# Optimization experiments

Measured on AMD Instinct MI355X. Metric: run time of the kernel, lower is better.

The kernel has to match this reference:

```python
import jax, jax.numpy as jnp
import numpy as np

S, I, H, FC, O = 16384, 64, 1024, 128, 1


def setup_inputs() -> dict:
    key = jax.random.key(0)
    ks = jax.random.split(key, 9)
    s_lstm = 1.0 / np.sqrt(H)
    return {
        "input_seq": jax.random.normal(ks[0], (S, I), jnp.float32),
        "W_ih": jax.random.uniform(ks[1], (4 * H, I), jnp.float32, -s_lstm, s_lstm),
        "W_hh": jax.random.uniform(ks[2], (4 * H, H), jnp.float32, -s_lstm, s_lstm),
        "b_ih": jax.random.uniform(ks[3], (4 * H,), jnp.float32, -s_lstm, s_lstm),
        "b_hh": jax.random.uniform(ks[4], (4 * H,), jnp.float32, -s_lstm, s_lstm),
        "fc1_w": jax.random.uniform(ks[5], (FC, H), jnp.float32, -s_lstm, s_lstm),
        "fc1_b": jax.random.uniform(ks[6], (FC,), jnp.float32, -s_lstm, s_lstm),
        "fc2_w": jax.random.uniform(ks[7], (O, FC), jnp.float32, -1.0 / np.sqrt(FC), 1.0 / np.sqrt(FC)),
        "fc2_b": jax.random.uniform(ks[8], (O,), jnp.float32, -1.0 / np.sqrt(FC), 1.0 / np.sqrt(FC)),
    }


def _lstm_scan(x, W_ih, W_hh, b_ih, b_hh):
    # PyTorch gate order: i, f, g, o. batch=1 collapsed; x: [S, I]
    xg = x @ W_ih.T + (b_ih + b_hh)  # precompute input-side gates: [S, 4H]

    def step(carry, xg_t):
        h, c = carry
        gates = xg_t + h @ W_hh.T
        i, f, g, o = jnp.split(gates, 4)
        i = jax.nn.sigmoid(i)
        f = jax.nn.sigmoid(f)
        g = jnp.tanh(g)
        o = jax.nn.sigmoid(o)
        c = f * c + i * g
        h = o * jnp.tanh(c)
        return (h, c), h

    h0 = jnp.zeros((H,), x.dtype)
    c0 = jnp.zeros((H,), x.dtype)
    _, hs = jax.lax.scan(step, (h0, c0), xg)
    return hs  # [S, H]


def reference(input_seq, W_ih, W_hh, b_ih, b_hh, fc1_w, fc1_b, fc2_w, fc2_b):
    hs = _lstm_scan(input_seq, W_ih, W_hh, b_ih, b_hh)       # [S, H]
    x = jax.nn.relu(hs)                                       # relu on LSTM outputs
    x = jax.nn.relu(x @ fc1_w.T + fc1_b)                      # [S, 128]
    x = x @ fc2_w.T + fc2_b                                   # [S, 1]
    return x[-1]                                              # [1]
```

## Files before the change

### kernel.cpp

```cpp
#include <hip/hip_runtime.h>
#include <hip/hip_fp16.h>


#define S_LEN 16384
#define I_DIM 64
#define H_DIM 1024
#define NBLK  64
#define NTHR  512

__device__ __forceinline__ float sigmoidf_(float x) { return 1.0f / (1.0f + __expf(-x)); }
__device__ __forceinline__ float tanh_fast(float x) { return 1.0f - 2.0f / (__expf(2.0f * x) + 1.0f); }
__device__ __forceinline__ float unpack_val(unsigned pk) {
    return __half2float(__ushort_as_half((unsigned short)(pk & 0xFFFFu)));
}

__global__ __launch_bounds__(NTHR, 2) void lstm_persistent(
    const float* __restrict__ xseq,
    const float* __restrict__ W_ih,
    const float* __restrict__ W_hh,
    const float* __restrict__ b_ih,
    const float* __restrict__ b_hh,
    unsigned* __restrict__ pairs)
{
    const int b    = blockIdx.x;
    const int tid  = threadIdx.x;
    const int w    = tid >> 6;
    const int c    = tid & 63;
    const int colA = 16 * b + 2 * w;

    __shared__ float4   h_stage[2][H_DIM / 4];
    __shared__ unsigned long long ld_pub[8];

    float4 wh[8][4];
    float  wi[8];
    float  bsum[8];
    #pragma unroll
    for (int r = 0; r < 8; ++r) {
        const int col = colA + (r >> 2);
        const int q   = r & 3;
        const size_t row = (size_t)q * H_DIM + col;
        const float4* wr = (const float4*)(W_hh + row * H_DIM);
        #pragma unroll
        for (int m = 0; m < 4; ++m) wh[r][m] = wr[m * 64 + c];
        wi[r]   = W_ih[row * I_DIM + c];
        bsum[r] = b_ih[row] + b_hh[row];
    }

    if (tid < H_DIM / 4) h_stage[0][tid] = make_float4(0.f, 0.f, 0.f, 0.f);
    if (tid < 8) ld_pub[tid] = 0ull;
    float cstA = 0.f, cstB = 0.f;
    float xv = xseq[c];
    const bool own = (tid >= 8 * b) && (tid < 8 * b + 8);
    __syncthreads();

    for (int t = 0; t < S_LEN; ++t) {
        const int cur = t & 1, nxt = cur ^ 1;
        const unsigned tag = (unsigned)(t + 1);

        float acc[8];
        #pragma unroll
        for (int r = 0; r < 8; ++r) acc[r] = wi[r] * xv;
        #pragma unroll
        for (int m = 0; m < 4; ++m) {
            const float4 hv = h_stage[cur][m * 64 + c];
            #pragma unroll
            for (int r = 0; r < 8; ++r) {
                acc[r] = fmaf(wh[r][m].x, hv.x, acc[r]);
                acc[r] = fmaf(wh[r][m].y, hv.y, acc[r]);
                acc[r] = fmaf(wh[r][m].z, hv.z, acc[r]);
                acc[r] = fmaf(wh[r][m].w, hv.w, acc[r]);
            }
        }

        if (t + 1 < S_LEN) xv = xseq[(size_t)(t + 1) * I_DIM + c];

        #pragma unroll
        for (int off = 32; off > 0; off >>= 1) {
            #pragma unroll
            for (int r = 0; r < 8; ++r) acc[r] += __shfl_xor(acc[r], off, 64);
        }

        const float igA = sigmoidf_(acc[0] + bsum[0]);
        const float fgA = sigmoidf_(acc[1] + bsum[1]);
        const float ggA = tanh_fast (acc[2] + bsum[2]);
        const float ogA = sigmoidf_(acc[3] + bsum[3]);
        cstA = fgA * cstA + igA * ggA;
        const float hA = ogA * tanh_fast(cstA);
        const float igB = sigmoidf_(acc[4] + bsum[4]);
        const float fgB = sigmoidf_(acc[5] + bsum[5]);
        const float ggB = tanh_fast (acc[6] + bsum[6]);
        const float ogB = sigmoidf_(acc[7] + bsum[7]);
        cstB = fgB * cstB + igB * ggB;
        const float hB = ogB * tanh_fast(cstB);

        const unsigned pkA = (tag << 16) | (unsigned)__half_as_ushort(__float2half(hA));
        const unsigned pkB = (tag << 16) | (unsigned)__half_as_ushort(__float2half(hB));
        if (c == 0) {
            const unsigned long long both = ((unsigned long long)pkB << 32) | pkA;
            __hip_atomic_store(&ld_pub[w], both,
                               __ATOMIC_RELAXED, __HIP_MEMORY_SCOPE_WORKGROUP);
        }

        if (w == 0 && c < 16) {
            const unsigned* mb = (const unsigned*)ld_pub;
            unsigned pk;
            for (;;) {
                pk = __hip_atomic_load(&mb[c], __ATOMIC_RELAXED,
                                       __HIP_MEMORY_SCOPE_WORKGROUP);
                if ((pk >> 16) == tag) break;
            }
            __hip_atomic_store(&pairs[(size_t)cur * H_DIM + 16 * b + c], pk,
                               __ATOMIC_RELAXED, __HIP_MEMORY_SCOPE_AGENT);
            ((float*)h_stage[nxt])[16 * b + c] = unpack_val(pk);
        }

        if (t == S_LEN - 1) break;

        if (!own) {
            const unsigned long long tag2 =
                ((unsigned long long)tag << 48) | ((unsigned long long)tag << 16);
            const unsigned long long* p =
                (const unsigned long long*)&pairs[(size_t)cur * H_DIM + 2 * tid];
            unsigned long long v;
            for (;;) {
                v = __hip_atomic_load(p, __ATOMIC_RELAXED, __HIP_MEMORY_SCOPE_AGENT);
                if (((v ^ tag2) & 0xFFFF0000FFFF0000ull) == 0ull) break;
                __builtin_amdgcn_s_sleep(1);
            }
            ((float2*)h_stage[nxt])[tid] =
                make_float2(unpack_val((unsigned)v), unpack_val((unsigned)(v >> 32)));
        }
        __syncthreads();
    }
}

__global__ __launch_bounds__(256) void fc_head(
    const unsigned* __restrict__ pairs,
    const float* __restrict__ fc1_w,
    const float* __restrict__ fc1_b,
    const float* __restrict__ fc2_w,
    const float* __restrict__ fc2_b,
    float* __restrict__ out)
{
    const int tid = threadIdx.x;
    __shared__ float4 hr4[H_DIM / 4];
    __shared__ float  partial[256];
    __shared__ float  r1[128];

    const uint4 pa = ((const uint4*)(pairs + H_DIM))[tid];
    float4 hv = make_float4(__half2float(__ushort_as_half((unsigned short)(pa.x & 0xFFFFu))),
                            __half2float(__ushort_as_half((unsigned short)(pa.y & 0xFFFFu))),
                            __half2float(__ushort_as_half((unsigned short)(pa.z & 0xFFFFu))),
                            __half2float(__ushort_as_half((unsigned short)(pa.w & 0xFFFFu))));
    hv.x = fmaxf(hv.x, 0.f); hv.y = fmaxf(hv.y, 0.f);
    hv.z = fmaxf(hv.z, 0.f); hv.w = fmaxf(hv.w, 0.f);
    hr4[tid] = hv;
    __syncthreads();

    const int row = tid & 127, half = tid >> 7;
    const float4* wrow = (const float4*)(fc1_w + (size_t)row * H_DIM) + half * 128;
    float a0 = 0.f, a1 = 0.f;
    #pragma unroll 4
    for (int i = 0; i < 128; i += 2) {
        const float4 w0 = wrow[i],     h0 = hr4[half * 128 + i];
        const float4 w1 = wrow[i + 1], h1 = hr4[half * 128 + i + 1];
        a0 += w0.x * h0.x + w0.y * h0.y + w0.z * h0.z + w0.w * h0.w;
        a1 += w1.x * h1.x + w1.y * h1.y + w1.z * h1.z + w1.w * h1.w;
    }
    partial[tid] = a0 + a1;
    __syncthreads();
    if (tid < 128) {
        const float s = partial[tid] + partial[tid + 128] + fc1_b[tid];
        r1[tid] = fmaxf(s, 0.f);
    }
    __syncthreads();
    if (tid < 64) {
        float v = r1[tid] * fc2_w[tid] + r1[tid + 64] * fc2_w[tid + 64];
        #pragma unroll
        for (int off = 32; off > 0; off >>= 1) v += __shfl_xor(v, off, 64);
        if (tid == 0) out[0] = v + fc2_b[0];
    }
}

extern "C" void kernel_launch(void* const* d_in, const int* in_sizes, int n_in,
                              void* d_out, int out_size, void* d_ws, size_t ws_size,
                              hipStream_t stream) {
    (void)in_sizes; (void)n_in; (void)out_size; (void)ws_size;
    const float* xseq  = (const float*)d_in[0];
    const float* W_ih  = (const float*)d_in[1];
    const float* W_hh  = (const float*)d_in[2];
    const float* b_ih  = (const float*)d_in[3];
    const float* b_hh  = (const float*)d_in[4];
    const float* fc1_w = (const float*)d_in[5];
    const float* fc1_b = (const float*)d_in[6];
    const float* fc2_w = (const float*)d_in[7];
    const float* fc2_b = (const float*)d_in[8];
    unsigned* pairs = (unsigned*)d_ws;

    lstm_persistent<<<NBLK, NTHR, 0, stream>>>(xseq, W_ih, W_hh, b_ih, b_hh, pairs);
    fc_head<<<1, 256, 0, stream>>>(pairs, fc1_w, fc1_b, fc2_w, fc2_b, (float*)d_out);
}
```

Baseline: 43.53 ms.

## Publish hidden pairs directly from each wave and drop spin sleep

Each wave's lane 0 now writes its packed pair of hidden values straight to the global exchange buffer and local staging. This removes the intra-block LDS mailbox and the wave-0 gather loop, taking one serialized hop out of every timestep's critical path. The cross-block spin loop also drops its s_sleep, so polling is more aggressive and memory traffic may rise. The W_hh register array is flattened to scalars behind an asm barrier, presumably to keep the weights resident in VGPRs.

New measurement: 73.68 ms. +69.3%, slower.

```diff
diff --git a/kernel.cpp b/kernel.cpp
--- a/kernel.cpp
+++ b/kernel.cpp
@@ -28,12 +28,11 @@
     const int c    = tid & 63;
     const int colA = 16 * b + 2 * w;
 
-    __shared__ float4   h_stage[2][H_DIM / 4];
-    __shared__ unsigned long long ld_pub[8];
+    __shared__ float4 h_stage[2][H_DIM / 4];
 
-    float4 wh[8][4];
-    float  wi[8];
-    float  bsum[8];
+    float wh[8][16];
+    float wi[8];
+    float bsum[8];
     #pragma unroll
     for (int r = 0; r < 8; ++r) {
         const int col = colA + (r >> 2);
@@ -41,13 +40,17 @@
         const size_t row = (size_t)q * H_DIM + col;
         const float4* wr = (const float4*)(W_hh + row * H_DIM);
         #pragma unroll
-        for (int m = 0; m < 4; ++m) wh[r][m] = wr[m * 64 + c];
+        for (int m = 0; m < 4; ++m) {
+            float4 v = wr[m * 64 + c];
+            asm volatile("" : "+v"(v.x), "+v"(v.y), "+v"(v.z), "+v"(v.w));
+            wh[r][4 * m + 0] = v.x; wh[r][4 * m + 1] = v.y;
+            wh[r][4 * m + 2] = v.z; wh[r][4 * m + 3] = v.w;
+        }
         wi[r]   = W_ih[row * I_DIM + c];
         bsum[r] = b_ih[row] + b_hh[row];
     }
 
     if (tid < H_DIM / 4) h_stage[0][tid] = make_float4(0.f, 0.f, 0.f, 0.f);
-    if (tid < 8) ld_pub[tid] = 0ull;
     float cstA = 0.f, cstB = 0.f;
     float xv = xseq[c];
     const bool own = (tid >= 8 * b) && (tid < 8 * b + 8);
@@ -65,10 +68,10 @@
             const float4 hv = h_stage[cur][m * 64 + c];
             #pragma unroll
             for (int r = 0; r < 8; ++r) {
-                acc[r] = fmaf(wh[r][m].x, hv.x, acc[r]);
-                acc[r] = fmaf(wh[r][m].y, hv.y, acc[r]);
-                acc[r] = fmaf(wh[r][m].z, hv.z, acc[r]);
-                acc[r] = fmaf(wh[r][m].w, hv.w, acc[r]);
+                acc[r] = fmaf(wh[r][4 * m + 0], hv.x, acc[r]);
+                acc[r] = fmaf(wh[r][4 * m + 1], hv.y, acc[r]);
+                acc[r] = fmaf(wh[r][4 * m + 2], hv.z, acc[r]);
+                acc[r] = fmaf(wh[r][4 * m + 3], hv.w, acc[r]);
             }
         }
 
@@ -97,21 +100,11 @@
         const unsigned pkB = (tag << 16) | (unsigned)__half_as_ushort(__float2half(hB));
         if (c == 0) {
             const unsigned long long both = ((unsigned long long)pkB << 32) | pkA;
-            __hip_atomic_store(&ld_pub[w], both,
-                               __ATOMIC_RELAXED, __HIP_MEMORY_SCOPE_WORKGROUP);
-        }
-
-        if (w == 0 && c < 16) {
-            const unsigned* mb = (const unsigned*)ld_pub;
-            unsigned pk;
-            for (;;) {
-                pk = __hip_atomic_load(&mb[c], __ATOMIC_RELAXED,
-                                       __HIP_MEMORY_SCOPE_WORKGROUP);
-                if ((pk >> 16) == tag) break;
-            }
-            __hip_atomic_store(&pairs[(size_t)cur * H_DIM + 16 * b + c], pk,
-                               __ATOMIC_RELAXED, __HIP_MEMORY_SCOPE_AGENT);
-            ((float*)h_stage[nxt])[16 * b + c] = unpack_val(pk);
+            __hip_atomic_store(
+                (unsigned long long*)&pairs[(size_t)cur * H_DIM + colA], both,
+                __ATOMIC_RELAXED, __HIP_MEMORY_SCOPE_AGENT);
+            ((float2*)h_stage[nxt])[8 * b + w] =
+                make_float2(unpack_val(pkA), unpack_val(pkB));
         }
 
         if (t == S_LEN - 1) break;
@@ -125,7 +118,6 @@
             for (;;) {
                 v = __hip_atomic_load(p, __ATOMIC_RELAXED, __HIP_MEMORY_SCOPE_AGENT);
                 if (((v ^ tag2) & 0xFFFF0000FFFF0000ull) == 0ull) break;
-                __builtin_amdgcn_s_sleep(1);
             }
             ((float2*)h_stage[nxt])[tid] =
                 make_float2(unpack_val((unsigned)v), unpack_val((unsigned)(v >> 32)));
```

## Single-buffer h_stage, stage x in LDS, replace spin mailbox with barrier

Applied to the files above, without the earlier changes.

Replaces the intra-block spin-wait mailbox with a plain LDS publish followed by __syncthreads, which lets h_stage drop from double to single buffer because a barrier now separates reads from writes. The next x row is prefetched into a double-buffered LDS stage by one wave, replacing the per-thread global load of x each step. The W_hh register loads get an asm barrier and an explicit waves_per_eu attribute so the weights stay resident in VGPRs. This adds one extra block-wide barrier per timestep, traded against the removed polling loop.

Measured after the change: 53.51 ms. +22.9%, slower.

```diff
diff --git a/kernel.cpp b/kernel.cpp
--- a/kernel.cpp
+++ b/kernel.cpp
@@ -14,7 +14,8 @@
     return __half2float(__ushort_as_half((unsigned short)(pk & 0xFFFFu)));
 }
 
-__global__ __launch_bounds__(NTHR, 2) void lstm_persistent(
+__global__ __launch_bounds__(NTHR) __attribute__((amdgpu_waves_per_eu(2, 2)))
+void lstm_persistent(
     const float* __restrict__ xseq,
     const float* __restrict__ W_ih,
     const float* __restrict__ W_hh,
@@ -28,8 +29,9 @@
     const int c    = tid & 63;
     const int colA = 16 * b + 2 * w;
 
-    __shared__ float4   h_stage[2][H_DIM / 4];
-    __shared__ unsigned long long ld_pub[8];
+    __shared__ float4   h_stage[H_DIM / 4];
+    __shared__ float    x_stage[2][I_DIM];
+    __shared__ unsigned pub[16];
 
     float4 wh[8][4];
     float  wi[8];
@@ -41,28 +43,36 @@
         const size_t row = (size_t)q * H_DIM + col;
         const float4* wr = (const float4*)(W_hh + row * H_DIM);
         #pragma unroll
-        for (int m = 0; m < 4; ++m) wh[r][m] = wr[m * 64 + c];
+        for (int m = 0; m < 4; ++m) {
+            float4 v = wr[m * 64 + c];
+            asm volatile("" : "+v"(v.x), "+v"(v.y), "+v"(v.z), "+v"(v.w));
+            wh[r][m] = v;
+        }
         wi[r]   = W_ih[row * I_DIM + c];
         bsum[r] = b_ih[row] + b_hh[row];
     }
 
-    if (tid < H_DIM / 4) h_stage[0][tid] = make_float4(0.f, 0.f, 0.f, 0.f);
-    if (tid < 8) ld_pub[tid] = 0ull;
+    if (tid < H_DIM / 4) h_stage[tid] = make_float4(0.f, 0.f, 0.f, 0.f);
+    if (tid < 16) ((float4*)x_stage[0])[tid] = ((const float4*)xseq)[tid];
     float cstA = 0.f, cstB = 0.f;
-    float xv = xseq[c];
     const bool own = (tid >= 8 * b) && (tid < 8 * b + 8);
     __syncthreads();
 
     for (int t = 0; t < S_LEN; ++t) {
-        const int cur = t & 1, nxt = cur ^ 1;
+        const int cur = t & 1;
         const unsigned tag = (unsigned)(t + 1);
 
+        if (w == 7 && c < 16 && t + 1 < S_LEN)
+            ((float4*)x_stage[(t + 1) & 1])[c] =
+                ((const float4*)(xseq + (size_t)(t + 1) * I_DIM))[c];
+
+        const float xv = x_stage[cur][c];
         float acc[8];
         #pragma unroll
         for (int r = 0; r < 8; ++r) acc[r] = wi[r] * xv;
         #pragma unroll
         for (int m = 0; m < 4; ++m) {
-            const float4 hv = h_stage[cur][m * 64 + c];
+            const float4 hv = h_stage[m * 64 + c];
             #pragma unroll
             for (int r = 0; r < 8; ++r) {
                 acc[r] = fmaf(wh[r][m].x, hv.x, acc[r]);
@@ -71,8 +81,6 @@
                 acc[r] = fmaf(wh[r][m].w, hv.w, acc[r]);
             }
         }
-
-        if (t + 1 < S_LEN) xv = xseq[(size_t)(t + 1) * I_DIM + c];
 
         #pragma unroll
         for (int off = 32; off > 0; off >>= 1) {
@@ -95,23 +103,15 @@
 
         const unsigned pkA = (tag << 16) | (unsigned)__half_as_ushort(__float2half(hA));
         const unsigned pkB = (tag << 16) | (unsigned)__half_as_ushort(__float2half(hB));
-        if (c == 0) {
-            const unsigned long long both = ((unsigned long long)pkB << 32) | pkA;
-            __hip_atomic_store(&ld_pub[w], both,
-                               __ATOMIC_RELAXED, __HIP_MEMORY_SCOPE_WORKGROUP);
-        }
+        if (c == 0) { pub[2 * w] = pkA; pub[2 * w + 1] = pkB; }
+
+        __syncthreads();
 
         if (w == 0 && c < 16) {
-            const unsigned* mb = (const unsigned*)ld_pub;
-            unsigned pk;
-            for (;;) {
-                pk = __hip_atomic_load(&mb[c], __ATOMIC_RELAXED,
-                                       __HIP_MEMORY_SCOPE_WORKGROUP);
-                if ((pk >> 16) == tag) break;
-            }
+            const unsigned pk = pub[c];
             __hip_atomic_store(&pairs[(size_t)cur * H_DIM + 16 * b + c], pk,
                                __ATOMIC_RELAXED, __HIP_MEMORY_SCOPE_AGENT);
-            ((float*)h_stage[nxt])[16 * b + c] = unpack_val(pk);
+            ((float*)h_stage)[16 * b + c] = unpack_val(pk);
         }
 
         if (t == S_LEN - 1) break;
@@ -127,7 +127,7 @@
                 if (((v ^ tag2) & 0xFFFF0000FFFF0000ull) == 0ull) break;
                 __builtin_amdgcn_s_sleep(1);
             }
-            ((float2*)h_stage[nxt])[tid] =
+            ((float2*)h_stage)[tid] =
                 make_float2(unpack_val((unsigned)v), unpack_val((unsigned)(v >> 32)));
         }
         __syncthreads();
```
